# Kernel optimization log

Hardware: AMD Instinct MI355X
Metric: run time of the kernel (lower is better)

The kernel has to match this reference:

```python
import jax, jax.numpy as jnp
import numpy as np

EPS = 1e-12  # matches torch F.normalize default eps
TEMP = 0.1


def _gram(x):
    # L2-normalize rows; for unit vectors 1 - 0.5*||xi-xj||^2 == xi . xj
    n = x / jnp.maximum(jnp.linalg.norm(x, axis=-1, keepdims=True), EPS)
    return n @ n.T  # [N, N]


def setup_inputs() -> dict:
    key = jax.random.key(0)
    k1, k2, k3, k4 = jax.random.split(key, 4)
    N, D = 4096, 512
    return {
        "fm_rgb": jax.random.normal(k1, (N, D), dtype=jnp.float32),
        "fm_depth": jax.random.normal(k2, (N, D), dtype=jnp.float32),
        "fm_ir": jax.random.normal(k3, (N, D), dtype=jnp.float32),
        "fm_t": jax.random.normal(k4, (N, D), dtype=jnp.float32),
    }


def reference(fm_rgb, fm_depth, fm_ir, fm_t):
    G_rgb = _gram(fm_rgb)
    G_depth = _gram(fm_depth)
    G_ir = _gram(fm_ir)
    G_t = _gram(fm_t)
    inv_t = 1.0 / TEMP
    loss_rgb = jnp.mean((G_t * inv_t - G_rgb * inv_t) ** 2)
    loss_depth = jnp.mean((G_t * inv_t - G_depth * inv_t) ** 2)
    loss_ir = jnp.mean((G_t * inv_t - G_ir * inv_t) ** 2)
    return loss_rgb + loss_depth + loss_ir
```

## Files before the change

kernel.cpp:

```cpp
#include <hip/hip_runtime.h>
#include <hip/hip_bf16.h>


typedef __attribute__((ext_vector_type(4))) float floatx4;
typedef __attribute__((ext_vector_type(2))) long long llx2;

#define N_ROWS 4096
#define DDIM   512
#define LOSS_SCALE 9.094947017729282e-11f

__device__ __forceinline__ const float* sel_mod(int mod, const float* a,
                                                const float* b, const float* c,
                                                const float* d) {
  return mod == 0 ? a : mod == 1 ? b : mod == 2 ? c : d;
}

__device__ __forceinline__ float bfr(float x) {
  __hip_bfloat16 h = __float2bfloat16(x);
  unsigned short u = *(unsigned short*)&h;
  return __uint_as_float(((unsigned int)u) << 16);
}

__global__ __launch_bounds__(512) void preprocess_kernel(
    const float* __restrict__ in0, const float* __restrict__ in1,
    const float* __restrict__ in2, const float* __restrict__ in3,
    unsigned char* __restrict__ nT8, float* __restrict__ out) {
  int mod = blockIdx.y;
  int k0 = blockIdx.x * 64;
  const float* X = sel_mod(mod, in0, in1, in2, in3) + (size_t)k0 * DDIM;

  if (blockIdx.x == 0 && blockIdx.y == 0 && threadIdx.x == 0)
    out[0] = 0.f;

  __shared__ float rsc[64];
  __shared__ unsigned int t8[512 * 17];

  int t = threadIdx.x;
  int a = t >> 5;
  int bg = t & 31;

  float4 v[4][4];
#pragma unroll
  for (int q = 0; q < 4; ++q)
#pragma unroll
    for (int p = 0; p < 4; ++p)
      v[q][p] = ((const float4*)(X + (size_t)(4 * a + q) * DDIM + p * 128))[bg];

  float ss[4];
#pragma unroll
  for (int q = 0; q < 4; ++q) {
    float acc = 0.f;
#pragma unroll
    for (int p = 0; p < 4; ++p) {
      float4 u = v[q][p];
      acc += u.x * u.x + u.y * u.y + u.z * u.z + u.w * u.w;
    }
    ss[q] = acc;
  }
#pragma unroll
  for (int off = 16; off > 0; off >>= 1)
#pragma unroll
    for (int q = 0; q < 4; ++q) ss[q] += __shfl_down(ss[q], off, 32);
  if (bg == 0) {
#pragma unroll
    for (int q = 0; q < 4; ++q)
      rsc[4 * a + q] = 16.0f / fmaxf(sqrtf(ss[q]), 1e-12f);
  }
  __syncthreads();

  float sc[4];
#pragma unroll
  for (int q = 0; q < 4; ++q) sc[q] = rsc[4 * a + q];

#pragma unroll
  for (int p = 0; p < 4; ++p)
#pragma unroll
    for (int j = 0; j < 4; ++j) {
      float f0 = bfr(((const float*)&v[0][p])[j] * sc[0]);
      float f1 = bfr(((const float*)&v[1][p])[j] * sc[1]);
      float f2 = bfr(((const float*)&v[2][p])[j] * sc[2]);
      float f3 = bfr(((const float*)&v[3][p])[j] * sc[3]);
      unsigned int pk = __builtin_amdgcn_cvt_pk_fp8_f32(f0, f1, 0, 0);
      pk = __builtin_amdgcn_cvt_pk_fp8_f32(f2, f3, pk, 1);
      t8[(p * 128 + bg * 4 + j) * 17 + a] = pk;
    }
  __syncthreads();

#pragma unroll
  for (int it = 0; it < 4; ++it) {
    int idx = it * 512 + t;
    int col = idx >> 2;
    int g = idx & 3;
    uint4 o;
    o.x = t8[col * 17 + g * 4 + 0];
    o.y = t8[col * 17 + g * 4 + 1];
    o.z = t8[col * 17 + g * 4 + 2];
    o.w = t8[col * 17 + g * 4 + 3];
    *(uint4*)(nT8 + ((size_t)(mod * DDIM + col)) * N_ROWS + k0 + g * 16) = o;
  }
}

__device__ __forceinline__ void stage_tiles1w(
    const unsigned char* __restrict__ Abase,
    const unsigned char* __restrict__ Bbase, int k0,
    unsigned char* ls, int lane) {
  int rr = lane >> 3;
  int s = lane & 7;
#pragma unroll
  for (int c = 0; c < 8; ++c) {
    int row = c * 8 + rr;
    int gc = s ^ ((row >> 1) & 7);
    const unsigned char* ga = Abase + (size_t)row * N_ROWS + k0 + gc * 16;
    __builtin_amdgcn_global_load_lds(
        (__attribute__((address_space(1))) void*)(void*)ga,
        (__attribute__((address_space(3))) void*)(void*)&ls[c * 1024],
        16, 0, 0);
  }
#pragma unroll
  for (int c = 0; c < 8; ++c) {
    int row = c * 8 + rr;
    int gc = s ^ ((row >> 1) & 7);
    const unsigned char* gb = Bbase + (size_t)row * N_ROWS + k0 + gc * 16;
    __builtin_amdgcn_global_load_lds(
        (__attribute__((address_space(1))) void*)(void*)gb,
        (__attribute__((address_space(3))) void*)(void*)&ls[8192 + c * 1024],
        16, 0, 0);
  }
}

__device__ __forceinline__ void compute_tiles1w(const unsigned char* ls,
                                                floatx4 acc[4][4], int lm,
                                                int lq) {
  llx2 A16[4][2], B16[4][2];
#pragma unroll
  for (int mi = 0; mi < 4; ++mi) {
    int row = mi * 16 + lm;
    int sw = (row >> 1) & 7;
    A16[mi][0] = *(const llx2*)&ls[row * 128 + ((lq * 2) ^ sw) * 16];
    A16[mi][1] = *(const llx2*)&ls[row * 128 + ((lq * 2 + 1) ^ sw) * 16];
  }
#pragma unroll
  for (int ni = 0; ni < 4; ++ni) {
    int row = ni * 16 + lm;
    int sw = (row >> 1) & 7;
    B16[ni][0] = *(const llx2*)&ls[8192 + row * 128 + ((lq * 2) ^ sw) * 16];
    B16[ni][1] =
        *(const llx2*)&ls[8192 + row * 128 + ((lq * 2 + 1) ^ sw) * 16];
  }
  __builtin_amdgcn_s_setprio(1);
#pragma unroll
  for (int ks = 0; ks < 4; ++ks) {
    int h = ks >> 1, e = ks & 1;
#pragma unroll
    for (int mi = 0; mi < 4; ++mi)
#pragma unroll
      for (int ni = 0; ni < 4; ++ni)
        acc[mi][ni] = __builtin_amdgcn_mfma_f32_16x16x32_fp8_fp8(
            A16[mi][h][e], B16[ni][h][e], acc[mi][ni], 0, 0, 0);
  }
  __builtin_amdgcn_s_setprio(0);
}

__global__ __launch_bounds__(64) void gram_frob_kernel(
    const unsigned char* __restrict__ nT8, float* __restrict__ out) {
  __shared__ __align__(16) unsigned char ls[4][16384];

  int bx = blockIdx.x;
  int pa_, pb_, ti, tj;
  float wgt;
  if (bx < 144) {
    int p = bx / 36;
    int t36 = bx - p * 36;
    int i = 0;
    while (t36 >= 8 - i) { t36 -= 8 - i; ++i; }
    ti = i;
    tj = i + t36;
    const int   sm[4] = {3, 0, 1, 2};
    const float sw_[4] = {3.f, 1.f, 1.f, 1.f};
    pa_ = sm[p];
    pb_ = sm[p];
    wgt = sw_[p] * (ti == tj ? 1.f : 2.f);
  } else {
    int r = bx - 144;
    int p = r >> 6;
    int t64 = r & 63;
    ti = t64 >> 3;
    tj = t64 & 7;
    pa_ = 3;
    pb_ = p;
    wgt = -2.f;
  }

  const unsigned char* Abase = nT8 + ((size_t)pa_ * DDIM + ti * 64) * N_ROWS;
  const unsigned char* Bbase = nT8 + ((size_t)pb_ * DDIM + tj * 64) * N_ROWS;

  int lane = threadIdx.x;
  int lm = lane & 15;
  int lq = lane >> 4;

  floatx4 zero = {0.f, 0.f, 0.f, 0.f};
  floatx4 acc[4][4];
#pragma unroll
  for (int mi = 0; mi < 4; ++mi)
#pragma unroll
    for (int ni = 0; ni < 4; ++ni) acc[mi][ni] = zero;

  unsigned char* p0 = ls[0];
  unsigned char* p1 = ls[1];
  unsigned char* p2 = ls[2];
  unsigned char* p3 = ls[3];
  stage_tiles1w(Abase, Bbase, 0, p0, lane);
  stage_tiles1w(Abase, Bbase, 128, p1, lane);
  stage_tiles1w(Abase, Bbase, 256, p2, lane);
  for (int i = 0; i < 30; ++i) {
    asm volatile("s_waitcnt vmcnt(32)" ::: "memory");
    __builtin_amdgcn_sched_barrier(0);
    if (i < 29)
      stage_tiles1w(Abase, Bbase, (i + 3) * 128, p3, lane);
    compute_tiles1w(p0, acc, lm, lq);
    unsigned char* tmp = p0; p0 = p1; p1 = p2; p2 = p3; p3 = tmp;
  }
  asm volatile("s_waitcnt vmcnt(16)" ::: "memory");
  __builtin_amdgcn_sched_barrier(0);
  compute_tiles1w(p0, acc, lm, lq);
  p0 = p1;
  asm volatile("s_waitcnt vmcnt(0)" ::: "memory");
  __builtin_amdgcn_sched_barrier(0);
  compute_tiles1w(p0, acc, lm, lq);

  float s = 0.f;
#pragma unroll
  for (int mi = 0; mi < 4; ++mi)
#pragma unroll
    for (int ni = 0; ni < 4; ++ni)
#pragma unroll
      for (int r = 0; r < 4; ++r) {
        float v = acc[mi][ni][r];
        s += v * v;
      }
#pragma unroll
  for (int off = 32; off > 0; off >>= 1) s += __shfl_down(s, off, 64);
  if (lane == 0) atomicAdd(out, wgt * LOSS_SCALE * s);
}

extern "C" void kernel_launch(void* const* d_in, const int* in_sizes, int n_in,
                              void* d_out, int out_size, void* d_ws, size_t ws_size,
                              hipStream_t stream) {
  const float* in_rgb   = (const float*)d_in[0];
  const float* in_depth = (const float*)d_in[1];
  const float* in_ir    = (const float*)d_in[2];
  const float* in_t     = (const float*)d_in[3];

  unsigned char* nT8 = (unsigned char*)d_ws;

  preprocess_kernel<<<dim3(64, 4), 512, 0, stream>>>(
      in_rgb, in_depth, in_ir, in_t, nT8, (float*)d_out);
  gram_frob_kernel<<<dim3(336), 64, 0, stream>>>(nT8, (float*)d_out);
}
```

Baseline: 108.8 us.

## Use 16x16x128 scaled fp8 MFMA with two-wave blocks and XCD-aware job mapping

Replaces the 16x16x32 fp8 MFMA with the gfx950 16x16x128 f8f6f4 scaled MFMA (unit scales), so a full 128-wide K chunk is consumed per instruction. Each block now runs two waves: one stages the A tile, the other the B tile, and each computes half of the N columns, with s_barrier synchronisation across the 4-stage LDS ring. Block indices are permuted so jobs spread round-robin across the XCDs. The extra cross-wave barriers add sync cost, and the per-wave accumulator footprint is halved.

```diff
diff --git a/kernel.cpp b/kernel.cpp
--- a/kernel.cpp
+++ b/kernel.cpp
@@ -4,6 +4,7 @@
 
 typedef __attribute__((ext_vector_type(4))) float floatx4;
 typedef __attribute__((ext_vector_type(2))) long long llx2;
+typedef __attribute__((ext_vector_type(8))) int intx8;
 
 #define N_ROWS 4096
 #define DDIM   512
@@ -100,77 +101,68 @@
   }
 }
 
-__device__ __forceinline__ void stage_tiles1w(
-    const unsigned char* __restrict__ Abase,
-    const unsigned char* __restrict__ Bbase, int k0,
-    unsigned char* ls, int lane) {
+__device__ __forceinline__ void stage_half(
+    const unsigned char* __restrict__ base, int k0, unsigned char* ls,
+    int lane) {
   int rr = lane >> 3;
   int s = lane & 7;
 #pragma unroll
   for (int c = 0; c < 8; ++c) {
     int row = c * 8 + rr;
     int gc = s ^ ((row >> 1) & 7);
-    const unsigned char* ga = Abase + (size_t)row * N_ROWS + k0 + gc * 16;
+    const unsigned char* g = base + (size_t)row * N_ROWS + k0 + gc * 16;
     __builtin_amdgcn_global_load_lds(
-        (__attribute__((address_space(1))) void*)(void*)ga,
+        (__attribute__((address_space(1))) void*)(void*)g,
         (__attribute__((address_space(3))) void*)(void*)&ls[c * 1024],
         16, 0, 0);
   }
-#pragma unroll
-  for (int c = 0; c < 8; ++c) {
-    int row = c * 8 + rr;
-    int gc = s ^ ((row >> 1) & 7);
-    const unsigned char* gb = Bbase + (size_t)row * N_ROWS + k0 + gc * 16;
-    __builtin_amdgcn_global_load_lds(
-        (__attribute__((address_space(1))) void*)(void*)gb,
-        (__attribute__((address_space(3))) void*)(void*)&ls[8192 + c * 1024],
-        16, 0, 0);
-  }
-}
-
-__device__ __forceinline__ void compute_tiles1w(const unsigned char* ls,
-                                                floatx4 acc[4][4], int lm,
-                                                int lq) {
-  llx2 A16[4][2], B16[4][2];
+}
+
+__device__ __forceinline__ void compute_w(const unsigned char* ls,
+                                          floatx4 acc[4][2], int wn, int lm,
+                                          int lq) {
+  intx8 A8[4], B8[2];
 #pragma unroll
   for (int mi = 0; mi < 4; ++mi) {
     int row = mi * 16 + lm;
     int sw = (row >> 1) & 7;
-    A16[mi][0] = *(const llx2*)&ls[row * 128 + ((lq * 2) ^ sw) * 16];
-    A16[mi][1] = *(const llx2*)&ls[row * 128 + ((lq * 2 + 1) ^ sw) * 16];
-  }
-#pragma unroll
-  for (int ni = 0; ni < 4; ++ni) {
-    int row = ni * 16 + lm;
+    *(llx2*)&A8[mi] = *(const llx2*)&ls[row * 128 + ((lq * 2) ^ sw) * 16];
+    *((llx2*)&A8[mi] + 1) =
+        *(const llx2*)&ls[row * 128 + ((lq * 2 + 1) ^ sw) * 16];
+  }
+#pragma unroll
+  for (int ni = 0; ni < 2; ++ni) {
+    int row = wn + ni * 16 + lm;
     int sw = (row >> 1) & 7;
-    B16[ni][0] = *(const llx2*)&ls[8192 + row * 128 + ((lq * 2) ^ sw) * 16];
-    B16[ni][1] =
+    *(llx2*)&B8[ni] =
+        *(const llx2*)&ls[8192 + row * 128 + ((lq * 2) ^ sw) * 16];
+    *((llx2*)&B8[ni] + 1) =
         *(const llx2*)&ls[8192 + row * 128 + ((lq * 2 + 1) ^ sw) * 16];
   }
   __builtin_amdgcn_s_setprio(1);
 #pragma unroll
-  for (int ks = 0; ks < 4; ++ks) {
-    int h = ks >> 1, e = ks & 1;
-#pragma unroll
-    for (int mi = 0; mi < 4; ++mi)
-#pragma unroll
-      for (int ni = 0; ni < 4; ++ni)
-        acc[mi][ni] = __builtin_amdgcn_mfma_f32_16x16x32_fp8_fp8(
-            A16[mi][h][e], B16[ni][h][e], acc[mi][ni], 0, 0, 0);
-  }
+  for (int mi = 0; mi < 4; ++mi)
+#pragma unroll
+    for (int ni = 0; ni < 2; ++ni)
+      acc[mi][ni] = __builtin_amdgcn_mfma_scale_f32_16x16x128_f8f6f4(
+          A8[mi], B8[ni], acc[mi][ni], 0, 0,
+          0, 0x7F, 0, 0x7F);
   __builtin_amdgcn_s_setprio(0);
 }
 
-__global__ __launch_bounds__(64) void gram_frob_kernel(
+__global__ __launch_bounds__(128) void gram_frob_kernel(
     const unsigned char* __restrict__ nT8, float* __restrict__ out) {
   __shared__ __align__(16) unsigned char ls[4][16384];
+  __shared__ float red[2];
 
   int bx = blockIdx.x;
+  int job = (bx & 7) * 42 + (bx >> 3);
+
   int pa_, pb_, ti, tj;
   float wgt;
-  if (bx < 144) {
-    int p = bx / 36;
-    int t36 = bx - p * 36;
+  if (job < 144) {
+    int p = job / 36;
+    int t36 = job - p * 36;
     int i = 0;
     while (t36 >= 8 - i) { t36 -= 8 - i; ++i; }
     ti = i;
@@ -181,7 +173,7 @@
     pb_ = sm[p];
     wgt = sw_[p] * (ti == tj ? 1.f : 2.f);
   } else {
-    int r = bx - 144;
+    int r = job - 144;
     int p = r >> 6;
     int t64 = r & 63;
     ti = t64 >> 3;
@@ -194,45 +186,50 @@
   const unsigned char* Abase = nT8 + ((size_t)pa_ * DDIM + ti * 64) * N_ROWS;
   const unsigned char* Bbase = nT8 + ((size_t)pb_ * DDIM + tj * 64) * N_ROWS;
 
-  int lane = threadIdx.x;
+  int t = threadIdx.x;
+  int w = t >> 6;
+  int lane = t & 63;
   int lm = lane & 15;
   int lq = lane >> 4;
+  int wn = w * 32;
+  const unsigned char* sbase = (w == 0) ? Abase : Bbase;
+  int soff = w * 8192;
 
   floatx4 zero = {0.f, 0.f, 0.f, 0.f};
-  floatx4 acc[4][4];
+  floatx4 acc[4][2];
 #pragma unroll
   for (int mi = 0; mi < 4; ++mi)
 #pragma unroll
-    for (int ni = 0; ni < 4; ++ni) acc[mi][ni] = zero;
-
-  unsigned char* p0 = ls[0];
-  unsigned char* p1 = ls[1];
-  unsigned char* p2 = ls[2];
-  unsigned char* p3 = ls[3];
-  stage_tiles1w(Abase, Bbase, 0, p0, lane);
-  stage_tiles1w(Abase, Bbase, 128, p1, lane);
-  stage_tiles1w(Abase, Bbase, 256, p2, lane);
-  for (int i = 0; i < 30; ++i) {
-    asm volatile("s_waitcnt vmcnt(32)" ::: "memory");
+    for (int ni = 0; ni < 2; ++ni) acc[mi][ni] = zero;
+
+  stage_half(sbase, 0, ls[0] + soff, lane);
+  stage_half(sbase, 128, ls[1] + soff, lane);
+  stage_half(sbase, 256, ls[2] + soff, lane);
+  for (int i = 0; i < 29; ++i) {
+    asm volatile("s_waitcnt vmcnt(16)" ::: "memory");
     __builtin_amdgcn_sched_barrier(0);
-    if (i < 29)
-      stage_tiles1w(Abase, Bbase, (i + 3) * 128, p3, lane);
-    compute_tiles1w(p0, acc, lm, lq);
-    unsigned char* tmp = p0; p0 = p1; p1 = p2; p2 = p3; p3 = tmp;
+    __builtin_amdgcn_s_barrier();
+    stage_half(sbase, (i + 3) * 128, ls[(i + 3) & 3] + soff, lane);
+    compute_w(ls[i & 3], acc, wn, lm, lq);
   }
   asm volatile("s_waitcnt vmcnt(16)" ::: "memory");
   __builtin_amdgcn_sched_barrier(0);
-  compute_tiles1w(p0, acc, lm, lq);
-  p0 = p1;
+  __builtin_amdgcn_s_barrier();
+  compute_w(ls[1], acc, wn, lm, lq);
+  asm volatile("s_waitcnt vmcnt(8)" ::: "memory");
+  __builtin_amdgcn_sched_barrier(0);
+  __builtin_amdgcn_s_barrier();
+  compute_w(ls[2], acc, wn, lm, lq);
   asm volatile("s_waitcnt vmcnt(0)" ::: "memory");
   __builtin_amdgcn_sched_barrier(0);
-  compute_tiles1w(p0, acc, lm, lq);
+  __builtin_amdgcn_s_barrier();
+  compute_w(ls[3], acc, wn, lm, lq);
 
   float s = 0.f;
 #pragma unroll
   for (int mi = 0; mi < 4; ++mi)
 #pragma unroll
-    for (int ni = 0; ni < 4; ++ni)
+    for (int ni = 0; ni < 2; ++ni)
 #pragma unroll
       for (int r = 0; r < 4; ++r) {
         float v = acc[mi][ni][r];
@@ -240,7 +237,10 @@
       }
 #pragma unroll
   for (int off = 32; off > 0; off >>= 1) s += __shfl_down(s, off, 64);
-  if (lane == 0) atomicAdd(out, wgt * LOSS_SCALE * s);
+  if (lane == 0) red[w] = s;
+  __syncthreads();
+  if (t == 0)
+    atomicAdd(out, wgt * LOSS_SCALE * (red[0] + red[1]));
 }
 
 extern "C" void kernel_launch(void* const* d_in, const int* in_sizes, int n_in,
@@ -255,5 +255,5 @@
 
   preprocess_kernel<<<dim3(64, 4), 512, 0, stream>>>(
       in_rgb, in_depth, in_ir, in_t, nT8, (float*)d_out);
-  gram_frob_kernel<<<dim3(336), 64, 0, stream>>>(nT8, (float*)d_out);
-}
+  gram_frob_kernel<<<dim3(336), 128, 0, stream>>>(nT8, (float*)d_out);
+}
```

Result: faster. 105.2 us (-3.3%).
